# Optimization experiments

Measured on AMD Instinct MI355X. Metric: run time of the kernel, lower is better.

Reference implementation:

```python
import jax, jax.numpy as jnp
import numpy as np

E = 32          # max_num_embodiments
STATE_DIM = 64  # max_state_dim
ACT_DIM = 32    # action_dim
HID = 1024      # hidden_size (state encoder hidden)
EMB = 1536      # input_embedding_dim (action encoder hidden_size)
B, T = 32, 32


def cat_linear(x, W, b, cat_ids):
    # x: (B,T,din), W: (E,din,dout), b: (E,dout), cat_ids: (B,)
    # faithful to: torch.bmm(x, W[cat_ids]) + b[cat_ids].unsqueeze(1)
    return jnp.einsum('btd,bdh->bth', x, W[cat_ids]) + b[cat_ids][:, None, :]


def sinusoidal_pos_encoding(t, dim):
    # t: (B,T) float timestep values -> (B,T,dim); standard transformer sinusoid
    half = dim // 2
    div = jnp.exp(-jnp.log(jnp.float32(10000.0)) * jnp.arange(half, dtype=jnp.float32) / half)
    ang = t[..., None] * div  # (B,T,half)
    return jnp.concatenate([jnp.sin(ang), jnp.cos(ang)], axis=-1)


def swish(x):
    return x * jax.nn.sigmoid(x)


def setup_inputs() -> dict:
    key = jax.random.key(0)
    ks = jax.random.split(key, 12)
    p = lambda k, shape: 0.02 * jax.random.normal(k, shape, dtype=jnp.float32)
    inp = {
        'state': jax.random.normal(ks[0], (B, 1, STATE_DIM), dtype=jnp.float32),
        'actions': jax.random.normal(ks[1], (B, T, ACT_DIM), dtype=jnp.float32),
        'timesteps': jax.random.randint(ks[2], (B,), 0, 1000, dtype=jnp.int32),
        'cat_ids': jax.random.randint(ks[3], (B,), 0, E, dtype=jnp.int32),
        # state_encoder: CategorySpecificMLP(E, STATE_DIM, HID, EMB)
        'se_W1': p(ks[4], (E, STATE_DIM, HID)), 'se_b1': jnp.zeros((E, HID), jnp.float32),
        'se_W2': p(ks[5], (E, HID, EMB)),       'se_b2': jnp.zeros((E, EMB), jnp.float32),
        # action_encoder: MultiEmbodimentActionEncoder(ACT_DIM, EMB, E)
        'ae_W1': p(ks[6], (E, ACT_DIM, EMB)),   'ae_b1': jnp.zeros((E, EMB), jnp.float32),
        'ae_W2': p(ks[7], (E, 2 * EMB, EMB)),   'ae_b2': jnp.zeros((E, EMB), jnp.float32),
        'ae_W3': p(ks[8], (E, EMB, EMB)),       'ae_b3': jnp.zeros((E, EMB), jnp.float32),
    }
    return inp


def reference(state, actions, timesteps, cat_ids,
              se_W1, se_b1, se_W2, se_b2,
              ae_W1, ae_b1, ae_W2, ae_b2, ae_W3, ae_b3):
    # state encoder: CategorySpecificMLP (relu between layers)
    h = jax.nn.relu(cat_linear(state, se_W1, se_b1, cat_ids))
    state_feat = cat_linear(h, se_W2, se_b2, cat_ids)  # (B,1,EMB)

    # action encoder: MultiEmbodimentActionEncoder
    t = jnp.broadcast_to(timesteps.astype(jnp.float32)[:, None], actions.shape[:2])  # (B,T)
    a_emb = cat_linear(actions, ae_W1, ae_b1, cat_ids)          # (B,T,EMB)
    tau_emb = sinusoidal_pos_encoding(t, EMB).astype(a_emb.dtype)
    x = jnp.concatenate([a_emb, tau_emb], axis=-1)              # (B,T,2*EMB)
    x = swish(cat_linear(x, ae_W2, ae_b2, cat_ids))
    action_emb = cat_linear(x, ae_W3, ae_b3, cat_ids)           # (B,T,EMB)

    # concat state + action tokens (as fed to the DiT downstream)
    return jnp.concatenate([state_feat, action_emb], axis=1)    # (B,T+1,EMB)
```

## Files before the change

kernel.cpp:

```cpp
#include <hip/hip_runtime.h>
#include <hip/hip_bf16.h>

#define B_   32
#define T_   32
#define E_   32
#define SD   64
#define AD   32
#define HID  1024
#define EMB  1536
#define K2   3072

typedef __attribute__((ext_vector_type(8))) short  bf16x8;
typedef __attribute__((ext_vector_type(8))) short  s16x8;
typedef __attribute__((ext_vector_type(4))) float  f32x4;

__device__ __forceinline__ unsigned short f2bf(float f) {
    unsigned u = __builtin_bit_cast(unsigned, f);
    u = u + 0x7fffu + ((u >> 16) & 1u);
    return (unsigned short)(u >> 16);
}

__device__ __forceinline__ float swishf(float y) {
    return y / (1.f + expf(-y));
}

__global__ __launch_bounds__(256) void k0(
    const float* __restrict__ state, const float* __restrict__ actions,
    const int* __restrict__ tsteps, const int* __restrict__ cat_ids,
    const float* __restrict__ se_W1, const float* __restrict__ se_b1,
    const float* __restrict__ ae_W1, const float* __restrict__ ae_b1,
    int* __restrict__ order, unsigned short* __restrict__ tau,
    float* __restrict__ h, unsigned short* __restrict__ aemb) {
    int bid = blockIdx.x, tid = threadIdx.x;

    if (bid == 0) {
        __shared__ int cats[B_];
        if (tid < B_) cats[tid] = cat_ids[tid];
        __syncthreads();
        if (tid == 0) {
            int idx = 0;
            for (int c = 0; c < E_; ++c)
                for (int b = 0; b < B_; ++b)
                    if (cats[b] == c) order[idx++] = b;
        }
        return;
    }
    if (bid <= B_) {
        int b = bid - 1;
        float t = (float)tsteps[b];
        const int half = EMB / 2;
        for (int i = tid; i < half; i += 256) {
            float div = expf((-logf(10000.0f) * (float)i) / (float)half);
            float ang = t * div;
            tau[b * EMB + i]        = f2bf(sinf(ang));
            tau[b * EMB + half + i] = f2bf(cosf(ang));
        }
        return;
    }
    if (bid <= 2 * B_) {
        int b = bid - (B_ + 1);
        int c = cat_ids[b];
        __shared__ float s[SD];
        if (tid < SD) s[tid] = state[b * SD + tid];
        __syncthreads();
        const float* W = se_W1 + (size_t)c * SD * HID;
        float acc[4];
#pragma unroll
        for (int r = 0; r < 4; ++r) acc[r] = se_b1[c * HID + tid + 256 * r];
        for (int k = 0; k < SD; ++k) {
            float sv = s[k];
#pragma unroll
            for (int r = 0; r < 4; ++r)
                acc[r] += sv * W[(size_t)k * HID + tid + 256 * r];
        }
#pragma unroll
        for (int r = 0; r < 4; ++r) {
            float v = acc[r];
            h[b * HID + tid + 256 * r] = v > 0.f ? v : 0.f;
        }
        return;
    }
    {
        int idx = bid - (2 * B_ + 1);
        int b = idx & 31, chunk = idx >> 5;
        int c = cat_ids[b];
        __shared__ float sa[T_ * AD];
#pragma unroll
        for (int r = 0; r < 4; ++r)
            sa[tid + 256 * r] = actions[b * T_ * AD + tid + 256 * r];
        __syncthreads();
        int n = chunk * 256 + tid;
        const float* W = ae_W1 + (size_t)c * AD * EMB + n;
        float bv = ae_b1[c * EMB + n];
        float acc[T_];
#pragma unroll
        for (int t = 0; t < T_; ++t) acc[t] = bv;
        for (int k = 0; k < AD; ++k) {
            float w = W[(size_t)k * EMB];
#pragma unroll
            for (int t = 0; t < T_; ++t) acc[t] += sa[t * AD + k] * w;
        }
#pragma unroll
        for (int t = 0; t < T_; ++t)
            aemb[((size_t)b * T_ + t) * EMB + n] = f2bf(acc[t]);
    }
}

__global__ __launch_bounds__(256) void k1(
    const int* __restrict__ order, const int* __restrict__ cat_ids,
    const unsigned short* __restrict__ aemb, const unsigned short* __restrict__ tau,
    const float* __restrict__ ae_W2, const float* __restrict__ ae_b2,
    const float* __restrict__ h, const float* __restrict__ se_W2,
    const float* __restrict__ se_b2,
    unsigned short* __restrict__ x3, float* __restrict__ out) {
    __shared__ float lds[4][32][64];
    int bid = blockIdx.x, tid = threadIdx.x;
    int wv = tid >> 6, lane = tid & 63;

    if (bid < (EMB / 64) * B_) {
        int slot = bid & 31, chunk = bid >> 5;
        int b = order[slot];
        int c = cat_ids[b];
        int cq = lane & 15, kg = lane >> 4;
        int ncol = chunk * 64 + 4 * cq;
        const float* Wb = ae_W2 + (size_t)c * K2 * EMB + ncol;

        f32x4 acc[2][4];
#pragma unroll
        for (int rf = 0; rf < 2; ++rf)
#pragma unroll
            for (int q = 0; q < 4; ++q) acc[rf][q] = (f32x4){0.f, 0.f, 0.f, 0.f};

        int kbeg = wv * 768;
        if (wv < 2) {
            const unsigned short* A0 = aemb + (size_t)b * T_ * EMB;
#pragma unroll 2
            for (int kk = 0; kk < 768; kk += 32) {
                int kb = kbeg + kk + kg * 8;
                f32x4 w[8];
#pragma unroll
                for (int j = 0; j < 8; ++j)
                    w[j] = *(const f32x4*)(Wb + (size_t)(kb + j) * EMB);
                bf16x8 bq[4];
#pragma unroll
                for (int q = 0; q < 4; ++q)
#pragma unroll
                    for (int j = 0; j < 8; ++j) bq[q][j] = (short)f2bf(w[j][q]);
                bf16x8 a0 = *(const bf16x8*)(A0 + (size_t)cq * EMB + kb);
                bf16x8 a1 = *(const bf16x8*)(A0 + (size_t)(cq + 16) * EMB + kb);
#pragma unroll
                for (int q = 0; q < 4; ++q) {
                    acc[0][q] = __builtin_amdgcn_mfma_f32_16x16x32_bf16(a0, bq[q], acc[0][q], 0, 0, 0);
                    acc[1][q] = __builtin_amdgcn_mfma_f32_16x16x32_bf16(a1, bq[q], acc[1][q], 0, 0, 0);
                }
            }
        } else {
            const unsigned short* TA = tau + (size_t)b * EMB;
#pragma unroll 2
            for (int kk = 0; kk < 768; kk += 32) {
                int kb = kbeg + kk + kg * 8;
                f32x4 w[8];
#pragma unroll
                for (int j = 0; j < 8; ++j)
                    w[j] = *(const f32x4*)(Wb + (size_t)(kb + j) * EMB);
                bf16x8 bq[4];
#pragma unroll
                for (int q = 0; q < 4; ++q)
#pragma unroll
                    for (int j = 0; j < 8; ++j) bq[q][j] = (short)f2bf(w[j][q]);
                bf16x8 a = *(const bf16x8*)(TA + (kb - EMB));
#pragma unroll
                for (int q = 0; q < 4; ++q) {
                    acc[0][q] = __builtin_amdgcn_mfma_f32_16x16x32_bf16(a, bq[q], acc[0][q], 0, 0, 0);
                    acc[1][q] = __builtin_amdgcn_mfma_f32_16x16x32_bf16(a, bq[q], acc[1][q], 0, 0, 0);
                }
            }
        }
#pragma unroll
        for (int rf = 0; rf < 2; ++rf)
#pragma unroll
            for (int r = 0; r < 4; ++r) {
                int row = kg * 4 + r + 16 * rf;
                f32x4 v;
#pragma unroll
                for (int q = 0; q < 4; ++q) v[q] = acc[rf][q][r];
                *(f32x4*)&lds[wv][row][4 * cq] = v;
            }
        __syncthreads();
        int row = tid >> 3, c0 = (tid & 7) * 8;
        int gcol = chunk * 64 + c0;
        s16x8 o;
#pragma unroll
        for (int j = 0; j < 8; ++j) {
            float y = lds[0][row][c0 + j] + lds[1][row][c0 + j]
                    + lds[2][row][c0 + j] + lds[3][row][c0 + j]
                    + ae_b2[c * EMB + gcol + j];
            o[j] = (short)f2bf(swishf(y));
        }
        *(s16x8*)(x3 + ((size_t)b * T_ + row) * EMB + gcol) = o;
    } else {
        int idx = bid - (EMB / 64) * B_;
        int slot = idx & 31, chunk = idx >> 5;
        int b = order[slot];
        int c = cat_ids[b];
        int n = chunk * 256 + 4 * lane;
        const float* W = se_W2 + (size_t)c * HID * EMB + n;
        const float* hb = h + (size_t)b * HID;
        f32x4 acc = {0.f, 0.f, 0.f, 0.f};
        int ke = 256 * wv + 256;
#pragma unroll 16
        for (int k = 256 * wv; k < ke; ++k) {
            f32x4 wvv = *(const f32x4*)(W + (size_t)k * EMB);
            float hk = hb[k];
            acc += hk * wvv;
        }
        float* l = (float*)lds;
        *(f32x4*)&l[(wv * 64 + lane) * 4] = acc;
        __syncthreads();
        if (tid < 64) {
            f32x4 s = *(f32x4*)&l[tid * 4];
#pragma unroll
            for (int w = 1; w < 4; ++w) s += *(f32x4*)&l[(w * 64 + tid) * 4];
            s += *(const f32x4*)(se_b2 + (size_t)c * EMB + chunk * 256 + 4 * tid);
            *(f32x4*)(out + ((size_t)b * 33) * EMB + chunk * 256 + 4 * tid) = s;
        }
    }
}

__global__ __launch_bounds__(256) void k2(
    const int* __restrict__ order, const int* __restrict__ cat_ids,
    const unsigned short* __restrict__ x3, const float* __restrict__ ae_W3,
    const float* __restrict__ ae_b3, float* __restrict__ out) {
    __shared__ float lds[4][32][64];
    int bid = blockIdx.x, tid = threadIdx.x;
    int wv = tid >> 6, lane = tid & 63;
    int slot = bid & 31, chunk = bid >> 5;
    int b = order[slot];
    int c = cat_ids[b];
    int cq = lane & 15, kg = lane >> 4;
    int ncol = chunk * 64 + 4 * cq;
    const float* Wb = ae_W3 + (size_t)c * EMB * EMB + ncol;
    const unsigned short* A0 = x3 + (size_t)b * T_ * EMB;

    f32x4 acc[2][4];
#pragma unroll
    for (int rf = 0; rf < 2; ++rf)
#pragma unroll
        for (int q = 0; q < 4; ++q) acc[rf][q] = (f32x4){0.f, 0.f, 0.f, 0.f};

    int kbeg = wv * 384;
#pragma unroll 2
    for (int kk = 0; kk < 384; kk += 32) {
        int kb = kbeg + kk + kg * 8;
        f32x4 w[8];
#pragma unroll
        for (int j = 0; j < 8; ++j)
            w[j] = *(const f32x4*)(Wb + (size_t)(kb + j) * EMB);
        bf16x8 bq[4];
#pragma unroll
        for (int q = 0; q < 4; ++q)
#pragma unroll
            for (int j = 0; j < 8; ++j) bq[q][j] = (short)f2bf(w[j][q]);
        bf16x8 a0 = *(const bf16x8*)(A0 + (size_t)cq * EMB + kb);
        bf16x8 a1 = *(const bf16x8*)(A0 + (size_t)(cq + 16) * EMB + kb);
#pragma unroll
        for (int q = 0; q < 4; ++q) {
            acc[0][q] = __builtin_amdgcn_mfma_f32_16x16x32_bf16(a0, bq[q], acc[0][q], 0, 0, 0);
            acc[1][q] = __builtin_amdgcn_mfma_f32_16x16x32_bf16(a1, bq[q], acc[1][q], 0, 0, 0);
        }
    }
#pragma unroll
    for (int rf = 0; rf < 2; ++rf)
#pragma unroll
        for (int r = 0; r < 4; ++r) {
            int row = kg * 4 + r + 16 * rf;
            f32x4 v;
#pragma unroll
            for (int q = 0; q < 4; ++q) v[q] = acc[rf][q][r];
            *(f32x4*)&lds[wv][row][4 * cq] = v;
        }
    __syncthreads();
    int row = tid >> 3, c0 = (tid & 7) * 8;
    int gcol = chunk * 64 + c0;
    f32x4 o0, o1;
#pragma unroll
    for (int j = 0; j < 4; ++j) {
        o0[j] = lds[0][row][c0 + j] + lds[1][row][c0 + j]
              + lds[2][row][c0 + j] + lds[3][row][c0 + j]
              + ae_b3[c * EMB + gcol + j];
        o1[j] = lds[0][row][c0 + 4 + j] + lds[1][row][c0 + 4 + j]
              + lds[2][row][c0 + 4 + j] + lds[3][row][c0 + 4 + j]
              + ae_b3[c * EMB + gcol + 4 + j];
    }
    float* orow = out + ((size_t)b * 33 + 1 + row) * EMB + gcol;
    *(f32x4*)orow = o0;
    *(f32x4*)(orow + 4) = o1;
}

extern "C" void kernel_launch(void* const* d_in, const int* in_sizes, int n_in,
                              void* d_out, int out_size, void* d_ws, size_t ws_size,
                              hipStream_t stream) {
    const float* state   = (const float*)d_in[0];
    const float* actions = (const float*)d_in[1];
    const int*   tsteps  = (const int*)d_in[2];
    const int*   cat_ids = (const int*)d_in[3];
    const float* se_W1 = (const float*)d_in[4];
    const float* se_b1 = (const float*)d_in[5];
    const float* se_W2 = (const float*)d_in[6];
    const float* se_b2 = (const float*)d_in[7];
    const float* ae_W1 = (const float*)d_in[8];
    const float* ae_b1 = (const float*)d_in[9];
    const float* ae_W2 = (const float*)d_in[10];
    const float* ae_b2 = (const float*)d_in[11];
    const float* ae_W3 = (const float*)d_in[12];
    const float* ae_b3 = (const float*)d_in[13];
    float* out = (float*)d_out;

    char* ws = (char*)d_ws;
    int*            order = (int*)(ws + 0);
    unsigned short* tau   = (unsigned short*)(ws + 256);
    float*          h     = (float*)(ws + 98560);
    unsigned short* aemb  = (unsigned short*)(ws + 229632);
    unsigned short* x3    = (unsigned short*)(ws + 3375360);

    k0<<<1 + 2 * B_ + (EMB / 256) * B_, 256, 0, stream>>>(
        state, actions, tsteps, cat_ids, se_W1, se_b1, ae_W1, ae_b1,
        order, tau, h, aemb);
    k1<<<(EMB / 64) * B_ + (EMB / 256) * B_, 256, 0, stream>>>(
        order, cat_ids, aemb, tau, ae_W2, ae_b2, h, se_W2, se_b2, x3, out);
    k2<<<(EMB / 64) * B_, 256, 0, stream>>>(order, cat_ids, x3, ae_W3, ae_b3, out);
}
```

Measured before the change: 214.4 us.

## Fuse three kernels into one persistent launch with per-batch atomic gates

Merges the three stage kernels into a single launch and orders the work with per-batch atomic counters, so a later-stage block only spin-waits until its own batch's inputs are ready. The aim is to remove inter-kernel launch gaps and full-grid barriers so stages for different batches can overlap. It also drops the category-sorted order for L2 weight reuse, adds a memset launch, and depends on producer blocks being scheduled before their consumers to avoid deadlock.

New measurement: 317.9 us. +48.3%, slower.

```diff
diff --git a/kernel.cpp b/kernel.cpp
--- a/kernel.cpp
+++ b/kernel.cpp
@@ -10,6 +10,17 @@
 #define EMB  1536
 #define K2   3072
 
+#define NB_AE   (6 * B_)
+#define NB_SH   B_
+#define NB_B1   ((EMB / 64) * B_)
+#define NB_SF   ((EMB / 256) * B_)
+#define NB_K2   ((EMB / 64) * B_)
+#define OFF_SH  NB_AE
+#define OFF_B1  (NB_AE + NB_SH)
+#define OFF_SF  (OFF_B1 + NB_B1)
+#define OFF_K2  (OFF_SF + NB_SF)
+#define NBLK    (OFF_K2 + NB_K2)
+
 typedef __attribute__((ext_vector_type(8))) short  bf16x8;
 typedef __attribute__((ext_vector_type(8))) short  s16x8;
 typedef __attribute__((ext_vector_type(4))) float  f32x4;
@@ -24,67 +35,50 @@
     return y / (1.f + expf(-y));
 }
 
-__global__ __launch_bounds__(256) void k0(
+__device__ __forceinline__ void gate_signal(int* g) {
+    __syncthreads();
+    if (threadIdx.x == 0)
+        __hip_atomic_fetch_add(g, 1, __ATOMIC_RELEASE, __HIP_MEMORY_SCOPE_AGENT);
+}
+
+__device__ __forceinline__ void gate_wait(const int* g, int target) {
+    if (threadIdx.x == 0) {
+        while (__hip_atomic_load(g, __ATOMIC_ACQUIRE, __HIP_MEMORY_SCOPE_AGENT) < target)
+            __builtin_amdgcn_s_sleep(8);
+    }
+    __syncthreads();
+}
+
+__global__ __launch_bounds__(256) void k_fused(
     const float* __restrict__ state, const float* __restrict__ actions,
     const int* __restrict__ tsteps, const int* __restrict__ cat_ids,
     const float* __restrict__ se_W1, const float* __restrict__ se_b1,
+    const float* __restrict__ se_W2, const float* __restrict__ se_b2,
     const float* __restrict__ ae_W1, const float* __restrict__ ae_b1,
-    int* __restrict__ order, unsigned short* __restrict__ tau,
-    float* __restrict__ h, unsigned short* __restrict__ aemb) {
+    const float* __restrict__ ae_W2, const float* __restrict__ ae_b2,
+    const float* __restrict__ ae_W3, const float* __restrict__ ae_b3,
+    int* __restrict__ gate_ae, int* __restrict__ gate_h, int* __restrict__ gate_x3,
+    unsigned short* __restrict__ tau, float* __restrict__ h,
+    unsigned short* __restrict__ aemb, unsigned short* __restrict__ x3,
+    float* __restrict__ out) {
+    __shared__ float lds[4][32][64];
     int bid = blockIdx.x, tid = threadIdx.x;
-
-    if (bid == 0) {
-        __shared__ int cats[B_];
-        if (tid < B_) cats[tid] = cat_ids[tid];
-        __syncthreads();
-        if (tid == 0) {
-            int idx = 0;
-            for (int c = 0; c < E_; ++c)
-                for (int b = 0; b < B_; ++b)
-                    if (cats[b] == c) order[idx++] = b;
-        }
-        return;
-    }
-    if (bid <= B_) {
-        int b = bid - 1;
-        float t = (float)tsteps[b];
-        const int half = EMB / 2;
-        for (int i = tid; i < half; i += 256) {
-            float div = expf((-logf(10000.0f) * (float)i) / (float)half);
-            float ang = t * div;
-            tau[b * EMB + i]        = f2bf(sinf(ang));
-            tau[b * EMB + half + i] = f2bf(cosf(ang));
-        }
-        return;
-    }
-    if (bid <= 2 * B_) {
-        int b = bid - (B_ + 1);
-        int c = cat_ids[b];
-        __shared__ float s[SD];
-        if (tid < SD) s[tid] = state[b * SD + tid];
-        __syncthreads();
-        const float* W = se_W1 + (size_t)c * SD * HID;
-        float acc[4];
-#pragma unroll
-        for (int r = 0; r < 4; ++r) acc[r] = se_b1[c * HID + tid + 256 * r];
-        for (int k = 0; k < SD; ++k) {
-            float sv = s[k];
-#pragma unroll
-            for (int r = 0; r < 4; ++r)
-                acc[r] += sv * W[(size_t)k * HID + tid + 256 * r];
-        }
-#pragma unroll
-        for (int r = 0; r < 4; ++r) {
-            float v = acc[r];
-            h[b * HID + tid + 256 * r] = v > 0.f ? v : 0.f;
-        }
-        return;
-    }
-    {
-        int idx = bid - (2 * B_ + 1);
-        int b = idx & 31, chunk = idx >> 5;
-        int c = cat_ids[b];
-        __shared__ float sa[T_ * AD];
+    int wv = tid >> 6, lane = tid & 63;
+
+    if (bid < NB_AE) {
+        int b = bid / 6, chunk = bid % 6;
+        int c = cat_ids[b];
+        if (chunk == 0) {
+            float t = (float)tsteps[b];
+            const int half = EMB / 2;
+            for (int i = tid; i < half; i += 256) {
+                float div = expf((-logf(10000.0f) * (float)i) / (float)half);
+                float ang = t * div;
+                tau[b * EMB + i]        = f2bf(sinf(ang));
+                tau[b * EMB + half + i] = f2bf(cosf(ang));
+            }
+        }
+        float* sa = (float*)lds;
 #pragma unroll
         for (int r = 0; r < 4; ++r)
             sa[tid + 256 * r] = actions[b * T_ * AD + tid + 256 * r];
@@ -103,27 +97,44 @@
 #pragma unroll
         for (int t = 0; t < T_; ++t)
             aemb[((size_t)b * T_ + t) * EMB + n] = f2bf(acc[t]);
-    }
-}
-
-__global__ __launch_bounds__(256) void k1(
-    const int* __restrict__ order, const int* __restrict__ cat_ids,
-    const unsigned short* __restrict__ aemb, const unsigned short* __restrict__ tau,
-    const float* __restrict__ ae_W2, const float* __restrict__ ae_b2,
-    const float* __restrict__ h, const float* __restrict__ se_W2,
-    const float* __restrict__ se_b2,
-    unsigned short* __restrict__ x3, float* __restrict__ out) {
-    __shared__ float lds[4][32][64];
-    int bid = blockIdx.x, tid = threadIdx.x;
-    int wv = tid >> 6, lane = tid & 63;
-
-    if (bid < (EMB / 64) * B_) {
-        int slot = bid & 31, chunk = bid >> 5;
-        int b = order[slot];
+        gate_signal(&gate_ae[b]);
+        return;
+    }
+
+    if (bid < OFF_B1) {
+        int b = bid - OFF_SH;
+        int c = cat_ids[b];
+        float* s = (float*)lds;
+        if (tid < SD) s[tid] = state[b * SD + tid];
+        __syncthreads();
+        const float* W = se_W1 + (size_t)c * SD * HID;
+        float acc[4];
+#pragma unroll
+        for (int r = 0; r < 4; ++r) acc[r] = se_b1[c * HID + tid + 256 * r];
+        for (int k = 0; k < SD; ++k) {
+            float sv = s[k];
+#pragma unroll
+            for (int r = 0; r < 4; ++r)
+                acc[r] += sv * W[(size_t)k * HID + tid + 256 * r];
+        }
+#pragma unroll
+        for (int r = 0; r < 4; ++r) {
+            float v = acc[r];
+            h[b * HID + tid + 256 * r] = v > 0.f ? v : 0.f;
+        }
+        gate_signal(&gate_h[b]);
+        return;
+    }
+
+    if (bid < OFF_SF) {
+        int idx = bid - OFF_B1;
+        int b = idx / 24, chunk = idx % 24;
         int c = cat_ids[b];
         int cq = lane & 15, kg = lane >> 4;
         int ncol = chunk * 64 + 4 * cq;
         const float* Wb = ae_W2 + (size_t)c * K2 * EMB + ncol;
+
+        gate_wait(&gate_ae[b], 6);
 
         f32x4 acc[2][4];
 #pragma unroll
@@ -198,11 +209,15 @@
             o[j] = (short)f2bf(swishf(y));
         }
         *(s16x8*)(x3 + ((size_t)b * T_ + row) * EMB + gcol) = o;
-    } else {
-        int idx = bid - (EMB / 64) * B_;
-        int slot = idx & 31, chunk = idx >> 5;
-        int b = order[slot];
-        int c = cat_ids[b];
+        gate_signal(&gate_x3[b]);
+        return;
+    }
+
+    if (bid < OFF_K2) {
+        int idx = bid - OFF_SF;
+        int b = idx & 31, chunk = idx >> 5;
+        int c = cat_ids[b];
+        gate_wait(&gate_h[b], 1);
         int n = chunk * 256 + 4 * lane;
         const float* W = se_W2 + (size_t)c * HID * EMB + n;
         const float* hb = h + (size_t)b * HID;
@@ -224,77 +239,74 @@
             s += *(const f32x4*)(se_b2 + (size_t)c * EMB + chunk * 256 + 4 * tid);
             *(f32x4*)(out + ((size_t)b * 33) * EMB + chunk * 256 + 4 * tid) = s;
         }
-    }
-}
-
-__global__ __launch_bounds__(256) void k2(
-    const int* __restrict__ order, const int* __restrict__ cat_ids,
-    const unsigned short* __restrict__ x3, const float* __restrict__ ae_W3,
-    const float* __restrict__ ae_b3, float* __restrict__ out) {
-    __shared__ float lds[4][32][64];
-    int bid = blockIdx.x, tid = threadIdx.x;
-    int wv = tid >> 6, lane = tid & 63;
-    int slot = bid & 31, chunk = bid >> 5;
-    int b = order[slot];
-    int c = cat_ids[b];
-    int cq = lane & 15, kg = lane >> 4;
-    int ncol = chunk * 64 + 4 * cq;
-    const float* Wb = ae_W3 + (size_t)c * EMB * EMB + ncol;
-    const unsigned short* A0 = x3 + (size_t)b * T_ * EMB;
-
-    f32x4 acc[2][4];
-#pragma unroll
-    for (int rf = 0; rf < 2; ++rf)
-#pragma unroll
-        for (int q = 0; q < 4; ++q) acc[rf][q] = (f32x4){0.f, 0.f, 0.f, 0.f};
-
-    int kbeg = wv * 384;
+        return;
+    }
+
+    {
+        int idx = bid - OFF_K2;
+        int b = idx / 24, chunk = idx % 24;
+        int c = cat_ids[b];
+        int cq = lane & 15, kg = lane >> 4;
+        int ncol = chunk * 64 + 4 * cq;
+        const float* Wb = ae_W3 + (size_t)c * EMB * EMB + ncol;
+
+        gate_wait(&gate_x3[b], 24);
+        const unsigned short* A0 = x3 + (size_t)b * T_ * EMB;
+
+        f32x4 acc[2][4];
+#pragma unroll
+        for (int rf = 0; rf < 2; ++rf)
+#pragma unroll
+            for (int q = 0; q < 4; ++q) acc[rf][q] = (f32x4){0.f, 0.f, 0.f, 0.f};
+
+        int kbeg = wv * 384;
 #pragma unroll 2
-    for (int kk = 0; kk < 384; kk += 32) {
-        int kb = kbeg + kk + kg * 8;
-        f32x4 w[8];
-#pragma unroll
-        for (int j = 0; j < 8; ++j)
-            w[j] = *(const f32x4*)(Wb + (size_t)(kb + j) * EMB);
-        bf16x8 bq[4];
-#pragma unroll
-        for (int q = 0; q < 4; ++q)
-#pragma unroll
-            for (int j = 0; j < 8; ++j) bq[q][j] = (short)f2bf(w[j][q]);
-        bf16x8 a0 = *(const bf16x8*)(A0 + (size_t)cq * EMB + kb);
-        bf16x8 a1 = *(const bf16x8*)(A0 + (size_t)(cq + 16) * EMB + kb);
-#pragma unroll
-        for (int q = 0; q < 4; ++q) {
-            acc[0][q] = __builtin_amdgcn_mfma_f32_16x16x32_bf16(a0, bq[q], acc[0][q], 0, 0, 0);
-            acc[1][q] = __builtin_amdgcn_mfma_f32_16x16x32_bf16(a1, bq[q], acc[1][q], 0, 0, 0);
-        }
-    }
-#pragma unroll
-    for (int rf = 0; rf < 2; ++rf)
-#pragma unroll
-        for (int r = 0; r < 4; ++r) {
-            int row = kg * 4 + r + 16 * rf;
-            f32x4 v;
-#pragma unroll
-            for (int q = 0; q < 4; ++q) v[q] = acc[rf][q][r];
-            *(f32x4*)&lds[wv][row][4 * cq] = v;
-        }
-    __syncthreads();
-    int row = tid >> 3, c0 = (tid & 7) * 8;
-    int gcol = chunk * 64 + c0;
-    f32x4 o0, o1;
-#pragma unroll
-    for (int j = 0; j < 4; ++j) {
-        o0[j] = lds[0][row][c0 + j] + lds[1][row][c0 + j]
-              + lds[2][row][c0 + j] + lds[3][row][c0 + j]
-              + ae_b3[c * EMB + gcol + j];
-        o1[j] = lds[0][row][c0 + 4 + j] + lds[1][row][c0 + 4 + j]
-              + lds[2][row][c0 + 4 + j] + lds[3][row][c0 + 4 + j]
-              + ae_b3[c * EMB + gcol + 4 + j];
-    }
-    float* orow = out + ((size_t)b * 33 + 1 + row) * EMB + gcol;
-    *(f32x4*)orow = o0;
-    *(f32x4*)(orow + 4) = o1;
+        for (int kk = 0; kk < 384; kk += 32) {
+            int kb = kbeg + kk + kg * 8;
+            f32x4 w[8];
+#pragma unroll
+            for (int j = 0; j < 8; ++j)
+                w[j] = *(const f32x4*)(Wb + (size_t)(kb + j) * EMB);
+            bf16x8 bq[4];
+#pragma unroll
+            for (int q = 0; q < 4; ++q)
+#pragma unroll
+                for (int j = 0; j < 8; ++j) bq[q][j] = (short)f2bf(w[j][q]);
+            bf16x8 a0 = *(const bf16x8*)(A0 + (size_t)cq * EMB + kb);
+            bf16x8 a1 = *(const bf16x8*)(A0 + (size_t)(cq + 16) * EMB + kb);
+#pragma unroll
+            for (int q = 0; q < 4; ++q) {
+                acc[0][q] = __builtin_amdgcn_mfma_f32_16x16x32_bf16(a0, bq[q], acc[0][q], 0, 0, 0);
+                acc[1][q] = __builtin_amdgcn_mfma_f32_16x16x32_bf16(a1, bq[q], acc[1][q], 0, 0, 0);
+            }
+        }
+#pragma unroll
+        for (int rf = 0; rf < 2; ++rf)
+#pragma unroll
+            for (int r = 0; r < 4; ++r) {
+                int row = kg * 4 + r + 16 * rf;
+                f32x4 v;
+#pragma unroll
+                for (int q = 0; q < 4; ++q) v[q] = acc[rf][q][r];
+                *(f32x4*)&lds[wv][row][4 * cq] = v;
+            }
+        __syncthreads();
+        int row = tid >> 3, c0 = (tid & 7) * 8;
+        int gcol = chunk * 64 + c0;
+        f32x4 o0, o1;
+#pragma unroll
+        for (int j = 0; j < 4; ++j) {
+            o0[j] = lds[0][row][c0 + j] + lds[1][row][c0 + j]
+                  + lds[2][row][c0 + j] + lds[3][row][c0 + j]
+                  + ae_b3[c * EMB + gcol + j];
+            o1[j] = lds[0][row][c0 + 4 + j] + lds[1][row][c0 + 4 + j]
+                  + lds[2][row][c0 + 4 + j] + lds[3][row][c0 + 4 + j]
+                  + ae_b3[c * EMB + gcol + 4 + j];
+        }
+        float* orow = out + ((size_t)b * 33 + 1 + row) * EMB + gcol;
+        *(f32x4*)orow = o0;
+        *(f32x4*)(orow + 4) = o1;
+    }
 }
 
 extern "C" void kernel_launch(void* const* d_in, const int* in_sizes, int n_in,
@@ -317,16 +329,18 @@
     float* out = (float*)d_out;
 
     char* ws = (char*)d_ws;
-    int*            order = (int*)(ws + 0);
-    unsigned short* tau   = (unsigned short*)(ws + 256);
-    float*          h     = (float*)(ws + 98560);
-    unsigned short* aemb  = (unsigned short*)(ws + 229632);
-    unsigned short* x3    = (unsigned short*)(ws + 3375360);
-
-    k0<<<1 + 2 * B_ + (EMB / 256) * B_, 256, 0, stream>>>(
-        state, actions, tsteps, cat_ids, se_W1, se_b1, ae_W1, ae_b1,
-        order, tau, h, aemb);
-    k1<<<(EMB / 64) * B_ + (EMB / 256) * B_, 256, 0, stream>>>(
-        order, cat_ids, aemb, tau, ae_W2, ae_b2, h, se_W2, se_b2, x3, out);
-    k2<<<(EMB / 64) * B_, 256, 0, stream>>>(order, cat_ids, x3, ae_W3, ae_b3, out);
-}
+    int*            gate_ae = (int*)(ws + 0);
+    int*            gate_h  = (int*)(ws + 128);
+    int*            gate_x3 = (int*)(ws + 256);
+    unsigned short* tau     = (unsigned short*)(ws + 512);
+    float*          h       = (float*)(ws + 98816);
+    unsigned short* aemb    = (unsigned short*)(ws + 229888);
+    unsigned short* x3      = (unsigned short*)(ws + 3375616);
+
+    hipMemsetAsync(ws, 0, 384, stream);
+    k_fused<<<NBLK, 256, 0, stream>>>(
+        state, actions, tsteps, cat_ids,
+        se_W1, se_b1, se_W2, se_b2,
+        ae_W1, ae_b1, ae_W2, ae_b2, ae_W3, ae_b3,
+        gate_ae, gate_h, gate_x3, tau, h, aemb, x3, out);
+}
```

## Group batch rows sharing an embodiment so each weight tile is loaded once

Applied to the files above, without the earlier changes.

Replaces the per-batch sorted order with groups of up to four batch rows that share the same category id. k1 and k2 then run one block per group and column chunk, loading and converting each weight tile once and applying it to every row in the group. This cuts repeated fp32 weight reads and bf16 conversions when categories repeat, and idle blocks exit early. In exchange each block holds four times as many accumulators, which raises register pressure (launch bounds now ask for 2 blocks per SM), the epilogue is serialized with extra barriers, and when categories are mostly distinct the grid is left with fewer useful blocks.

Result: slower. 513.0 us (+139.3%).

```diff
diff --git a/kernel.cpp b/kernel.cpp
--- a/kernel.cpp
+++ b/kernel.cpp
@@ -9,6 +9,7 @@
 #define HID  1024
 #define EMB  1536
 #define K2   3072
+#define GMAX 4
 
 typedef __attribute__((ext_vector_type(8))) short  bf16x8;
 typedef __attribute__((ext_vector_type(8))) short  s16x8;
@@ -29,19 +30,30 @@
     const int* __restrict__ tsteps, const int* __restrict__ cat_ids,
     const float* __restrict__ se_W1, const float* __restrict__ se_b1,
     const float* __restrict__ ae_W1, const float* __restrict__ ae_b1,
-    int* __restrict__ order, unsigned short* __restrict__ tau,
+    int* __restrict__ grp, unsigned short* __restrict__ tau,
     float* __restrict__ h, unsigned short* __restrict__ aemb) {
     int bid = blockIdx.x, tid = threadIdx.x;
 
     if (bid == 0) {
-        __shared__ int cats[B_];
-        if (tid < B_) cats[tid] = cat_ids[tid];
-        __syncthreads();
         if (tid == 0) {
-            int idx = 0;
-            for (int c = 0; c < E_; ++c)
+            int cats[B_];
+            for (int b = 0; b < B_; ++b) cats[b] = cat_ids[b];
+            int ng = 0;
+            for (int c = 0; c < E_; ++c) {
+                int tmp[B_], cnt = 0;
                 for (int b = 0; b < B_; ++b)
-                    if (cats[b] == c) order[idx++] = b;
+                    if (cats[b] == c) tmp[cnt++] = b;
+                int i = 0;
+                while (i < cnt) {
+                    int take = cnt - i; if (take > GMAX) take = GMAX;
+                    int* G = grp + 1 + ng * 6;
+                    G[0] = c; G[1] = take;
+                    for (int s = 0; s < GMAX; ++s)
+                        G[2 + s] = tmp[i + (s < take ? s : take - 1)];
+                    i += take; ++ng;
+                }
+            }
+            grp[0] = ng;
         }
         return;
     }
@@ -106,9 +118,9 @@
     }
 }
 
-__global__ __launch_bounds__(256) void k1(
-    const int* __restrict__ order, const int* __restrict__ cat_ids,
-    const unsigned short* __restrict__ aemb, const unsigned short* __restrict__ tau,
+__global__ __launch_bounds__(256, 2) void k1(
+    const int* __restrict__ grp, const unsigned short* __restrict__ aemb,
+    const unsigned short* __restrict__ tau,
     const float* __restrict__ ae_W2, const float* __restrict__ ae_b2,
     const float* __restrict__ h, const float* __restrict__ se_W2,
     const float* __restrict__ se_b2,
@@ -116,25 +128,30 @@
     __shared__ float lds[4][32][64];
     int bid = blockIdx.x, tid = threadIdx.x;
     int wv = tid >> 6, lane = tid & 63;
-
-    if (bid < (EMB / 64) * B_) {
-        int slot = bid & 31, chunk = bid >> 5;
-        int b = order[slot];
-        int c = cat_ids[b];
+    int ng = grp[0];
+
+    if (bid < 24 * B_) {
+        int g = bid / 24, chunk = bid % 24;
+        if (g >= ng) return;
+        const int* G = grp + 1 + g * 6;
+        int c = G[0], cnt = G[1];
+        int b0 = G[2], b1 = G[3], b2i = G[4], b3 = G[5];
+        int bs[GMAX] = {b0, b1, b2i, b3};
+
         int cq = lane & 15, kg = lane >> 4;
         int ncol = chunk * 64 + 4 * cq;
         const float* Wb = ae_W2 + (size_t)c * K2 * EMB + ncol;
 
-        f32x4 acc[2][4];
-#pragma unroll
-        for (int rf = 0; rf < 2; ++rf)
-#pragma unroll
-            for (int q = 0; q < 4; ++q) acc[rf][q] = (f32x4){0.f, 0.f, 0.f, 0.f};
+        f32x4 acc[GMAX][2][4];
+#pragma unroll
+        for (int s = 0; s < GMAX; ++s)
+#pragma unroll
+            for (int rf = 0; rf < 2; ++rf)
+#pragma unroll
+                for (int q = 0; q < 4; ++q) acc[s][rf][q] = (f32x4){0.f, 0.f, 0.f, 0.f};
 
         int kbeg = wv * 768;
         if (wv < 2) {
-            const unsigned short* A0 = aemb + (size_t)b * T_ * EMB;
-#pragma unroll 2
             for (int kk = 0; kk < 768; kk += 32) {
                 int kb = kbeg + kk + kg * 8;
                 f32x4 w[8];
@@ -146,17 +163,21 @@
                 for (int q = 0; q < 4; ++q)
 #pragma unroll
                     for (int j = 0; j < 8; ++j) bq[q][j] = (short)f2bf(w[j][q]);
-                bf16x8 a0 = *(const bf16x8*)(A0 + (size_t)cq * EMB + kb);
-                bf16x8 a1 = *(const bf16x8*)(A0 + (size_t)(cq + 16) * EMB + kb);
-#pragma unroll
-                for (int q = 0; q < 4; ++q) {
-                    acc[0][q] = __builtin_amdgcn_mfma_f32_16x16x32_bf16(a0, bq[q], acc[0][q], 0, 0, 0);
-                    acc[1][q] = __builtin_amdgcn_mfma_f32_16x16x32_bf16(a1, bq[q], acc[1][q], 0, 0, 0);
+#pragma unroll
+                for (int s = 0; s < GMAX; ++s) {
+                    if (s < cnt) {
+                        const unsigned short* A0 = aemb + (size_t)bs[s] * T_ * EMB;
+                        bf16x8 a0 = *(const bf16x8*)(A0 + (size_t)cq * EMB + kb);
+                        bf16x8 a1 = *(const bf16x8*)(A0 + (size_t)(cq + 16) * EMB + kb);
+#pragma unroll
+                        for (int q = 0; q < 4; ++q) {
+                            acc[s][0][q] = __builtin_amdgcn_mfma_f32_16x16x32_bf16(a0, bq[q], acc[s][0][q], 0, 0, 0);
+                            acc[s][1][q] = __builtin_amdgcn_mfma_f32_16x16x32_bf16(a1, bq[q], acc[s][1][q], 0, 0, 0);
+                        }
+                    }
                 }
             }
         } else {
-            const unsigned short* TA = tau + (size_t)b * EMB;
-#pragma unroll 2
             for (int kk = 0; kk < 768; kk += 32) {
                 int kb = kbeg + kk + kg * 8;
                 f32x4 w[8];
@@ -168,88 +189,122 @@
                 for (int q = 0; q < 4; ++q)
 #pragma unroll
                     for (int j = 0; j < 8; ++j) bq[q][j] = (short)f2bf(w[j][q]);
-                bf16x8 a = *(const bf16x8*)(TA + (kb - EMB));
-#pragma unroll
-                for (int q = 0; q < 4; ++q) {
-                    acc[0][q] = __builtin_amdgcn_mfma_f32_16x16x32_bf16(a, bq[q], acc[0][q], 0, 0, 0);
-                    acc[1][q] = __builtin_amdgcn_mfma_f32_16x16x32_bf16(a, bq[q], acc[1][q], 0, 0, 0);
-                }
-            }
-        }
-#pragma unroll
-        for (int rf = 0; rf < 2; ++rf)
-#pragma unroll
-            for (int r = 0; r < 4; ++r) {
-                int row = kg * 4 + r + 16 * rf;
-                f32x4 v;
-#pragma unroll
-                for (int q = 0; q < 4; ++q) v[q] = acc[rf][q][r];
-                *(f32x4*)&lds[wv][row][4 * cq] = v;
-            }
-        __syncthreads();
-        int row = tid >> 3, c0 = (tid & 7) * 8;
-        int gcol = chunk * 64 + c0;
-        s16x8 o;
-#pragma unroll
-        for (int j = 0; j < 8; ++j) {
-            float y = lds[0][row][c0 + j] + lds[1][row][c0 + j]
-                    + lds[2][row][c0 + j] + lds[3][row][c0 + j]
-                    + ae_b2[c * EMB + gcol + j];
-            o[j] = (short)f2bf(swishf(y));
-        }
-        *(s16x8*)(x3 + ((size_t)b * T_ + row) * EMB + gcol) = o;
-    } else {
-        int idx = bid - (EMB / 64) * B_;
-        int slot = idx & 31, chunk = idx >> 5;
-        int b = order[slot];
-        int c = cat_ids[b];
+#pragma unroll
+                for (int s = 0; s < GMAX; ++s) {
+                    if (s < cnt) {
+                        bf16x8 a = *(const bf16x8*)(tau + (size_t)bs[s] * EMB + (kb - EMB));
+#pragma unroll
+                        for (int q = 0; q < 4; ++q) {
+                            acc[s][0][q] = __builtin_amdgcn_mfma_f32_16x16x32_bf16(a, bq[q], acc[s][0][q], 0, 0, 0);
+                            acc[s][1][q] = __builtin_amdgcn_mfma_f32_16x16x32_bf16(a, bq[q], acc[s][1][q], 0, 0, 0);
+                        }
+                    }
+                }
+            }
+        }
+#pragma unroll
+        for (int s = 0; s < GMAX; ++s) {
+            if (s < cnt) {
+                __syncthreads();
+#pragma unroll
+                for (int rf = 0; rf < 2; ++rf)
+#pragma unroll
+                    for (int r = 0; r < 4; ++r) {
+                        int row = kg * 4 + r + 16 * rf;
+                        f32x4 v;
+#pragma unroll
+                        for (int q = 0; q < 4; ++q) v[q] = acc[s][rf][q][r];
+                        *(f32x4*)&lds[wv][row][4 * cq] = v;
+                    }
+                __syncthreads();
+                int row = tid >> 3, c0 = (tid & 7) * 8;
+                int gcol = chunk * 64 + c0;
+                s16x8 o;
+#pragma unroll
+                for (int j = 0; j < 8; ++j) {
+                    float y = lds[0][row][c0 + j] + lds[1][row][c0 + j]
+                            + lds[2][row][c0 + j] + lds[3][row][c0 + j]
+                            + ae_b2[c * EMB + gcol + j];
+                    o[j] = (short)f2bf(swishf(y));
+                }
+                *(s16x8*)(x3 + ((size_t)bs[s] * T_ + row) * EMB + gcol) = o;
+            }
+        }
+        return;
+    }
+
+    {
+        int idx = bid - 24 * B_;
+        int g = idx / 6, chunk = idx % 6;
+        if (g >= ng) return;
+        const int* G = grp + 1 + g * 6;
+        int c = G[0], cnt = G[1];
+        int bs[GMAX] = {G[2], G[3], G[4], G[5]};
+
         int n = chunk * 256 + 4 * lane;
         const float* W = se_W2 + (size_t)c * HID * EMB + n;
-        const float* hb = h + (size_t)b * HID;
-        f32x4 acc = {0.f, 0.f, 0.f, 0.f};
+        const float* hb[GMAX];
+#pragma unroll
+        for (int s = 0; s < GMAX; ++s) hb[s] = h + (size_t)bs[s] * HID;
+
+        f32x4 acc[GMAX];
+#pragma unroll
+        for (int s = 0; s < GMAX; ++s) acc[s] = (f32x4){0.f, 0.f, 0.f, 0.f};
         int ke = 256 * wv + 256;
-#pragma unroll 16
+#pragma unroll 8
         for (int k = 256 * wv; k < ke; ++k) {
             f32x4 wvv = *(const f32x4*)(W + (size_t)k * EMB);
-            float hk = hb[k];
-            acc += hk * wvv;
+#pragma unroll
+            for (int s = 0; s < GMAX; ++s)
+                if (s < cnt) acc[s] += hb[s][k] * wvv;
         }
         float* l = (float*)lds;
-        *(f32x4*)&l[(wv * 64 + lane) * 4] = acc;
+#pragma unroll
+        for (int s = 0; s < GMAX; ++s)
+            if (s < cnt) *(f32x4*)&l[((wv * GMAX + s) * 64 + lane) * 4] = acc[s];
         __syncthreads();
-        if (tid < 64) {
-            f32x4 s = *(f32x4*)&l[tid * 4];
-#pragma unroll
-            for (int w = 1; w < 4; ++w) s += *(f32x4*)&l[(w * 64 + tid) * 4];
-            s += *(const f32x4*)(se_b2 + (size_t)c * EMB + chunk * 256 + 4 * tid);
-            *(f32x4*)(out + ((size_t)b * 33) * EMB + chunk * 256 + 4 * tid) = s;
-        }
-    }
-}
-
-__global__ __launch_bounds__(256) void k2(
-    const int* __restrict__ order, const int* __restrict__ cat_ids,
-    const unsigned short* __restrict__ x3, const float* __restrict__ ae_W3,
-    const float* __restrict__ ae_b3, float* __restrict__ out) {
+        int s = tid >> 6;
+        if (s < cnt) {
+            f32x4 sum = *(f32x4*)&l[((0 * GMAX + s) * 64 + lane) * 4];
+#pragma unroll
+            for (int w = 1; w < 4; ++w)
+                sum += *(f32x4*)&l[((w * GMAX + s) * 64 + lane) * 4];
+            sum += *(const f32x4*)(se_b2 + (size_t)c * EMB + chunk * 256 + 4 * lane);
+            *(f32x4*)(out + ((size_t)bs[s] * 33) * EMB + chunk * 256 + 4 * lane) = sum;
+        }
+    }
+}
+
+__global__ __launch_bounds__(256, 2) void k2(
+    const int* __restrict__ grp, const unsigned short* __restrict__ x3,
+    const float* __restrict__ ae_W3, const float* __restrict__ ae_b3,
+    float* __restrict__ out) {
     __shared__ float lds[4][32][64];
     int bid = blockIdx.x, tid = threadIdx.x;
     int wv = tid >> 6, lane = tid & 63;
-    int slot = bid & 31, chunk = bid >> 5;
-    int b = order[slot];
-    int c = cat_ids[b];
+    int ng = grp[0];
+    int g = bid / 24, chunk = bid % 24;
+    if (g >= ng) return;
+    const int* G = grp + 1 + g * 6;
+    int c = G[0], cnt = G[1];
+    int bs[GMAX] = {G[2], G[3], G[4], G[5]};
+
     int cq = lane & 15, kg = lane >> 4;
     int ncol = chunk * 64 + 4 * cq;
     const float* Wb = ae_W3 + (size_t)c * EMB * EMB + ncol;
-    const unsigned short* A0 = x3 + (size_t)b * T_ * EMB;
-
-    f32x4 acc[2][4];
-#pragma unroll
-    for (int rf = 0; rf < 2; ++rf)
-#pragma unroll
-        for (int q = 0; q < 4; ++q) acc[rf][q] = (f32x4){0.f, 0.f, 0.f, 0.f};
+    const unsigned short* A0s[GMAX];
+#pragma unroll
+    for (int s = 0; s < GMAX; ++s) A0s[s] = x3 + (size_t)bs[s] * T_ * EMB;
+
+    f32x4 acc[GMAX][2][4];
+#pragma unroll
+    for (int s = 0; s < GMAX; ++s)
+#pragma unroll
+        for (int rf = 0; rf < 2; ++rf)
+#pragma unroll
+            for (int q = 0; q < 4; ++q) acc[s][rf][q] = (f32x4){0.f, 0.f, 0.f, 0.f};
 
     int kbeg = wv * 384;
-#pragma unroll 2
     for (int kk = 0; kk < 384; kk += 32) {
         int kb = kbeg + kk + kg * 8;
         f32x4 w[8];
@@ -261,40 +316,51 @@
         for (int q = 0; q < 4; ++q)
 #pragma unroll
             for (int j = 0; j < 8; ++j) bq[q][j] = (short)f2bf(w[j][q]);
-        bf16x8 a0 = *(const bf16x8*)(A0 + (size_t)cq * EMB + kb);
-        bf16x8 a1 = *(const bf16x8*)(A0 + (size_t)(cq + 16) * EMB + kb);
-#pragma unroll
-        for (int q = 0; q < 4; ++q) {
-            acc[0][q] = __builtin_amdgcn_mfma_f32_16x16x32_bf16(a0, bq[q], acc[0][q], 0, 0, 0);
-            acc[1][q] = __builtin_amdgcn_mfma_f32_16x16x32_bf16(a1, bq[q], acc[1][q], 0, 0, 0);
-        }
-    }
-#pragma unroll
-    for (int rf = 0; rf < 2; ++rf)
-#pragma unroll
-        for (int r = 0; r < 4; ++r) {
-            int row = kg * 4 + r + 16 * rf;
-            f32x4 v;
-#pragma unroll
-            for (int q = 0; q < 4; ++q) v[q] = acc[rf][q][r];
-            *(f32x4*)&lds[wv][row][4 * cq] = v;
-        }
-    __syncthreads();
-    int row = tid >> 3, c0 = (tid & 7) * 8;
-    int gcol = chunk * 64 + c0;
-    f32x4 o0, o1;
-#pragma unroll
-    for (int j = 0; j < 4; ++j) {
-        o0[j] = lds[0][row][c0 + j] + lds[1][row][c0 + j]
-              + lds[2][row][c0 + j] + lds[3][row][c0 + j]
-              + ae_b3[c * EMB + gcol + j];
-        o1[j] = lds[0][row][c0 + 4 + j] + lds[1][row][c0 + 4 + j]
-              + lds[2][row][c0 + 4 + j] + lds[3][row][c0 + 4 + j]
-              + ae_b3[c * EMB + gcol + 4 + j];
-    }
-    float* orow = out + ((size_t)b * 33 + 1 + row) * EMB + gcol;
-    *(f32x4*)orow = o0;
-    *(f32x4*)(orow + 4) = o1;
+#pragma unroll
+        for (int s = 0; s < GMAX; ++s) {
+            if (s < cnt) {
+                bf16x8 a0 = *(const bf16x8*)(A0s[s] + (size_t)cq * EMB + kb);
+                bf16x8 a1 = *(const bf16x8*)(A0s[s] + (size_t)(cq + 16) * EMB + kb);
+#pragma unroll
+                for (int q = 0; q < 4; ++q) {
+                    acc[s][0][q] = __builtin_amdgcn_mfma_f32_16x16x32_bf16(a0, bq[q], acc[s][0][q], 0, 0, 0);
+                    acc[s][1][q] = __builtin_amdgcn_mfma_f32_16x16x32_bf16(a1, bq[q], acc[s][1][q], 0, 0, 0);
+                }
+            }
+        }
+    }
+#pragma unroll
+    for (int s = 0; s < GMAX; ++s) {
+        if (s < cnt) {
+            __syncthreads();
+#pragma unroll
+            for (int rf = 0; rf < 2; ++rf)
+#pragma unroll
+                for (int r = 0; r < 4; ++r) {
+                    int row = kg * 4 + r + 16 * rf;
+                    f32x4 v;
+#pragma unroll
+                    for (int q = 0; q < 4; ++q) v[q] = acc[s][rf][q][r];
+                    *(f32x4*)&lds[wv][row][4 * cq] = v;
+                }
+            __syncthreads();
+            int row = tid >> 3, c0 = (tid & 7) * 8;
+            int gcol = chunk * 64 + c0;
+            f32x4 o0, o1;
+#pragma unroll
+            for (int j = 0; j < 4; ++j) {
+                o0[j] = lds[0][row][c0 + j] + lds[1][row][c0 + j]
+                      + lds[2][row][c0 + j] + lds[3][row][c0 + j]
+                      + ae_b3[c * EMB + gcol + j];
+                o1[j] = lds[0][row][c0 + 4 + j] + lds[1][row][c0 + 4 + j]
+                      + lds[2][row][c0 + 4 + j] + lds[3][row][c0 + 4 + j]
+                      + ae_b3[c * EMB + gcol + 4 + j];
+            }
+            float* orow = out + ((size_t)bs[s] * 33 + 1 + row) * EMB + gcol;
+            *(f32x4*)orow = o0;
+            *(f32x4*)(orow + 4) = o1;
+        }
+    }
 }
 
 extern "C" void kernel_launch(void* const* d_in, const int* in_sizes, int n_in,
@@ -317,16 +383,16 @@
     float* out = (float*)d_out;
 
     char* ws = (char*)d_ws;
-    int*            order = (int*)(ws + 0);
-    unsigned short* tau   = (unsigned short*)(ws + 256);
-    float*          h     = (float*)(ws + 98560);
-    unsigned short* aemb  = (unsigned short*)(ws + 229632);
-    unsigned short* x3    = (unsigned short*)(ws + 3375360);
+    int*            grp  = (int*)(ws + 0);
+    unsigned short* tau  = (unsigned short*)(ws + 1024);
+    float*          h    = (float*)(ws + 99328);
+    unsigned short* aemb = (unsigned short*)(ws + 230400);
+    unsigned short* x3   = (unsigned short*)(ws + 3376128);
 
     k0<<<1 + 2 * B_ + (EMB / 256) * B_, 256, 0, stream>>>(
         state, actions, tsteps, cat_ids, se_W1, se_b1, ae_W1, ae_b1,
-        order, tau, h, aemb);
-    k1<<<(EMB / 64) * B_ + (EMB / 256) * B_, 256, 0, stream>>>(
-        order, cat_ids, aemb, tau, ae_W2, ae_b2, h, se_W2, se_b2, x3, out);
-    k2<<<(EMB / 64) * B_, 256, 0, stream>>>(order, cat_ids, x3, ae_W3, ae_b3, out);
-}
+        grp, tau, h, aemb);
+    k1<<<24 * B_ + 6 * B_, 256, 0, stream>>>(
+        grp, aemb, tau, ae_W2, ae_b2, h, se_W2, se_b2, x3, out);
+    k2<<<24 * B_, 256, 0, stream>>>(grp, x3, ae_W3, ae_b3, out);
+}
```
